# Performance work log

Measured on AMD Instinct MI355X. Metric: run time of the kernel, lower is better.

## Reference

```python
import jax, jax.numpy as jnp
import numpy as np

B, T, D, H = 4, 4096, 1024, 1024

def log_g(x):
    # log of g(x) = where(x>=0, x+0.5, sigmoid(x)), computed stably in log-space
    return jnp.where(x >= 0, jnp.log(jax.nn.relu(x) + 0.5), -jax.nn.softplus(-x))

def setup_inputs() -> dict:
    key = jax.random.key(0)
    ks = jax.random.split(key, 8)
    s = 1.0 / np.sqrt(D)
    return {
        "x":   jax.random.normal(ks[0], (B, T, D), dtype=jnp.float32),
        "h_0": jax.random.normal(ks[1], (B, H),    dtype=jnp.float32),
        "Wf":  jax.random.uniform(ks[2], (H, D), minval=-s, maxval=s, dtype=jnp.float32),
        "bf":  jax.random.uniform(ks[3], (H,),   minval=-s, maxval=s, dtype=jnp.float32),
        "Wi":  jax.random.uniform(ks[4], (H, D), minval=-s, maxval=s, dtype=jnp.float32),
        "bi":  jax.random.uniform(ks[5], (H,),   minval=-s, maxval=s, dtype=jnp.float32),
        "Wh":  jax.random.uniform(ks[6], (H, D), minval=-s, maxval=s, dtype=jnp.float32),
        "bh":  jax.random.uniform(ks[7], (H,),   minval=-s, maxval=s, dtype=jnp.float32),
    }

def reference(x, h_0, Wf, bf, Wi, bi, Wh, bh):
    # Gate pre-activations: (B, T, H)
    zf = jnp.einsum('btd,hd->bth', x, Wf) + bf
    zi = jnp.einsum('btd,hd->bth', x, Wi) + bi
    zh = jnp.einsum('btd,hd->bth', x, Wh) + bh

    # Normalized gates in log space: log f' = -softplus(diff), log i' = -softplus(-diff)
    diff = jax.nn.softplus(-zf) - jax.nn.softplus(-zi)
    log_f = -jax.nn.softplus(diff)
    log_i = -jax.nn.softplus(-diff)
    log_tilde_h = log_g(zh)

    log_h0 = log_g(h_0)[:, None, :]                               # (B, 1, H)
    log_values = jnp.concatenate([log_h0, log_i + log_tilde_h], axis=1)  # (B, T+1, H)

    # Log-space parallel scan: h_t = f_t h_{t-1} + v_t
    a_star = jnp.cumsum(log_f, axis=1)                            # (B, T, H)
    a_star_pad = jnp.pad(a_star, ((0, 0), (1, 0), (0, 0)))        # (B, T+1, H)
    log_h = a_star_pad + jax.lax.cumlogsumexp(log_values - a_star_pad, axis=1)
    return jnp.exp(log_h[:, 1:, :])                               # (B, T, H)
```

## Files before the change

### kernel.cpp

```cpp
#include <hip/hip_runtime.h>
#include <stdint.h>

#define BB 4
#define TT 4096
#define DD 1024
#define HH 1024
#define MM (BB * TT)
#define NC 128
#define CL (TT / NC)

typedef __bf16 bf16x8 __attribute__((ext_vector_type(8)));
typedef short  s16x8  __attribute__((ext_vector_type(8)));
typedef float  f32x4  __attribute__((ext_vector_type(4)));
typedef float  f32x16 __attribute__((ext_vector_type(16)));


__device__ __forceinline__ unsigned short f2bf(float f) {
    unsigned u = __float_as_uint(f);
    u += 0x7fffu + ((u >> 16) & 1u);
    return (unsigned short)(u >> 16);
}

__device__ __forceinline__ float bf2f(unsigned short u) {
    return __uint_as_float(((unsigned)u) << 16);
}

__device__ __forceinline__ float g_fn(float x) {
    return (x >= 0.f) ? (x + 0.5f) : 1.0f / (1.0f + __expf(-x));
}

__device__ __forceinline__ f32x16 mfma32(s16x8 a, s16x8 b, f32x16 c) {
    return __builtin_amdgcn_mfma_f32_32x32x16_bf16(
        __builtin_bit_cast(bf16x8, a), __builtin_bit_cast(bf16x8, b), c, 0, 0, 0);
}

__device__ __forceinline__ void async_copy16(const void* gsrc, void* ldst) {
    __builtin_amdgcn_global_load_lds(
        reinterpret_cast<__attribute__((address_space(1))) unsigned int*>(
            reinterpret_cast<uintptr_t>(gsrc)),
        reinterpret_cast<__attribute__((address_space(3))) unsigned int*>(
            reinterpret_cast<uintptr_t>(ldst)),
        16, 0, 0);
}


__global__ void cast_all(const float* __restrict__ x,
                         const float* __restrict__ Wf,
                         const float* __restrict__ Wi,
                         const float* __restrict__ Wh,
                         unsigned short* __restrict__ xb,
                         unsigned short* __restrict__ Wb) {
    const int NX = MM * DD / 4;
    int i = blockIdx.x * 256 + threadIdx.x;
    if (i < NX) {
        float4 v = reinterpret_cast<const float4*>(x)[i];
        ushort4 o;
        o.x = f2bf(v.x); o.y = f2bf(v.y); o.z = f2bf(v.z); o.w = f2bf(v.w);
        reinterpret_cast<ushort4*>(xb)[i] = o;
    } else {
        int j = i - NX;
        if (j < 3 * 262144) {
            int which = j >> 18, k = j & 262143;
            const float* s = (which == 0) ? Wf : ((which == 1) ? Wi : Wh);
            float4 v = reinterpret_cast<const float4*>(s)[k];
            ushort4 o;
            o.x = f2bf(v.x); o.y = f2bf(v.y); o.z = f2bf(v.z); o.w = f2bf(v.w);
            reinterpret_cast<ushort4*>(Wb)[(which << 18) + k] = o;
        }
    }
}


#define ISSUE(NB) do {                                                        \
    _Pragma("unroll")                                                         \
    for (int j = 0; j < 4; ++j)                                               \
        async_copy16(gptrA[j], smem + (NB) * 16384 + loffA[j]);               \
    _Pragma("unroll")                                                         \
    for (int j = 0; j < 3; ++j)                                               \
        async_copy16(gptrB[j], smem + 32768 + (NB) * 12288 + loffB[j]);       \
    _Pragma("unroll")                                                         \
    for (int j = 0; j < 4; ++j) gptrA[j] += 32;                               \
    _Pragma("unroll")                                                         \
    for (int j = 0; j < 3; ++j) gptrB[j] += 32;                               \
} while (0)

#define COMPUTE(CB) do {                                                      \
    const char* Ab = smem + (CB) * 16384;                                     \
    const char* Bb = smem + 32768 + (CB) * 12288;                             \
    _Pragma("unroll")                                                         \
    for (int ks = 0; ks < 2; ++ks) {                                          \
        const int col = c0 ^ (ks << 5);                                       \
        s16x8 a0 = *reinterpret_cast<const s16x8*>(Ab + arowb + col);         \
        s16x8 a1 = *reinterpret_cast<const s16x8*>(Ab + arowb + 2048 + col);  \
        s16x8 a2 = *reinterpret_cast<const s16x8*>(Ab + arowb + 4096 + col);  \
        s16x8 a3 = *reinterpret_cast<const s16x8*>(Ab + arowb + 6144 + col);  \
        s16x8 b0 = *reinterpret_cast<const s16x8*>(Bb + browb + col);         \
        s16x8 b1 = *reinterpret_cast<const s16x8*>(Bb + browb + 4096 + col);  \
        s16x8 b2 = *reinterpret_cast<const s16x8*>(Bb + browb + 8192 + col);  \
        acc[0][0] = mfma32(a0, b0, acc[0][0]);                                \
        acc[1][0] = mfma32(a0, b1, acc[1][0]);                                \
        acc[2][0] = mfma32(a0, b2, acc[2][0]);                                \
        acc[0][1] = mfma32(a1, b0, acc[0][1]);                                \
        acc[1][1] = mfma32(a1, b1, acc[1][1]);                                \
        acc[2][1] = mfma32(a1, b2, acc[2][1]);                                \
        acc[0][2] = mfma32(a2, b0, acc[0][2]);                                \
        acc[1][2] = mfma32(a2, b1, acc[1][2]);                                \
        acc[2][2] = mfma32(a2, b2, acc[2][2]);                                \
        acc[0][3] = mfma32(a3, b0, acc[0][3]);                                \
        acc[1][3] = mfma32(a3, b1, acc[1][3]);                                \
        acc[2][3] = mfma32(a3, b2, acc[2][3]);                                \
    }                                                                         \
} while (0)

#define STEP(CB, NB, LAST) do {                                               \
    if (!(LAST)) {                                                            \
        ISSUE(NB);                                                            \
        asm volatile("s_waitcnt vmcnt(7)" ::: "memory");                      \
    } else {                                                                  \
        asm volatile("s_waitcnt vmcnt(0)" ::: "memory");                      \
    }                                                                         \
    __builtin_amdgcn_s_barrier();                                             \
    COMPUTE(CB);                                                              \
    asm volatile("s_waitcnt lgkmcnt(0)" ::: "memory");                        \
    __builtin_amdgcn_s_barrier();                                             \
} while (0)

__global__ __launch_bounds__(256, 2) void gemm_gates(
    const unsigned short* __restrict__ xb,
    const unsigned short* __restrict__ Wb,
    const float* __restrict__ bf_p, const float* __restrict__ bi_p,
    const float* __restrict__ bh_p,
    unsigned short* __restrict__ F, unsigned short* __restrict__ V) {
    __shared__ char smem[57344];

    const int tid  = threadIdx.x;
    const int wave = tid >> 6;
    const int lane = tid & 63;

    const int bi  = blockIdx.x;
    const int xcd = bi & 7;
    const int jj  = bi >> 3;
    const int bm  = ((jj & 7) << 3) | xcd;
    const int bh  = jj >> 3;

    const int pm   = wave >> 1;
    const int ph   = wave & 1;

    const unsigned short* gptrA[4];
    const unsigned short* gptrB[3];
    int loffA[4], loffB[3];
#pragma unroll
    for (int j = 0; j < 4; ++j) {
        int s = wave + j * 4;
        int gch = (lane & 3) ^ ((lane >> 3) & 3) ^ ((s * 2 + (lane >> 5)) & 3);
        int row = bm * 256 + s * 16 + (lane >> 2);
        gptrA[j] = xb + (size_t)row * DD + gch * 8;
        loffA[j] = s * 1024;
    }
#pragma unroll
    for (int j = 0; j < 3; ++j) {
        int s = wave + j * 4;
        int gch = (lane & 3) ^ ((lane >> 3) & 3) ^ ((s * 2 + (lane >> 5)) & 3);
        int row = (s >> 2) * HH + bh * 64 + (s & 3) * 16 + (lane >> 2);
        gptrB[j] = Wb + (size_t)row * DD + gch * 8;
        loffB[j] = s * 1024;
    }

    const int c0 = (((lane >> 5) ^ ((lane >> 1) & 3) ^ ((lane >> 3) & 3)) << 4);
    const int arowb = (pm * 128 + (lane & 31)) * 64;
    const int browb = (ph * 32 + (lane & 31)) * 64;

    f32x16 acc[3][4];
#pragma unroll
    for (int g = 0; g < 3; ++g)
#pragma unroll
        for (int mt = 0; mt < 4; ++mt)
            acc[g][mt] = (f32x16)(0.f);

    ISSUE(0);
    for (int t = 0; t < 15; ++t) {
        STEP(0, 1, 0);
        STEP(1, 0, 0);
    }
    STEP(0, 1, 0);
    STEP(1, 0, 1);

    const int h   = bh * 64 + ph * 32 + (lane & 31);
    const float bfs = bf_p[h], bis = bi_p[h], bhs = bh_p[h];
    const int mb  = bm * 256 + pm * 128 + ((lane >> 5) << 2);
#pragma unroll
    for (int mt = 0; mt < 4; ++mt) {
#pragma unroll
        for (int r = 0; r < 16; ++r) {
            const int m = mb + mt * 32 + (r & 3) + ((r >> 2) << 3);
            float zf = acc[0][mt][r] + bfs;
            float zi = acc[1][mt][r] + bis;
            float zh = acc[2][mt][r] + bhs;
            float ea = __expf(fminf(-zf, 60.f));
            float eb = __expf(fminf(-zi, 60.f));
            float s  = __builtin_amdgcn_rcpf(2.f + ea + eb);
            float fv = (1.f + eb) * s;
            float iv = (1.f + ea) * s;
            float gg = (zh >= 0.f) ? (zh + 0.5f)
                                   : __builtin_amdgcn_rcpf(1.f + __expf(-zh));
            size_t o = (size_t)m * HH + h;
            F[o] = f2bf(fv);
            V[o] = f2bf(iv * gg);
        }
    }
}


__global__ void scan1_kernel(const unsigned short* __restrict__ F,
                             const unsigned short* __restrict__ V,
                             float* __restrict__ Fc, float* __restrict__ Vc) {
    const int bx = blockIdx.x, tid = threadIdx.x;
    const int c = bx & (NC - 1), b = bx >> 7;
    const ushort4* F4 = (const ushort4*)F;
    const ushort4* V4 = (const ushort4*)V;
    size_t base = ((size_t)(b * TT + c * CL) * HH) / 4 + tid;
    float4 Fp = {1.f, 1.f, 1.f, 1.f}, hv = {0.f, 0.f, 0.f, 0.f};
#pragma unroll 8
    for (int s = 0; s < CL; ++s) {
        ushort4 fu = F4[base + (size_t)s * (HH / 4)];
        ushort4 vu = V4[base + (size_t)s * (HH / 4)];
        hv.x = fmaf(bf2f(fu.x), hv.x, bf2f(vu.x)); Fp.x *= bf2f(fu.x);
        hv.y = fmaf(bf2f(fu.y), hv.y, bf2f(vu.y)); Fp.y *= bf2f(fu.y);
        hv.z = fmaf(bf2f(fu.z), hv.z, bf2f(vu.z)); Fp.z *= bf2f(fu.z);
        hv.w = fmaf(bf2f(fu.w), hv.w, bf2f(vu.w)); Fp.w *= bf2f(fu.w);
    }
    size_t ci = ((size_t)(b * NC + c) * HH) / 4 + tid;
    ((float4*)Fc)[ci] = Fp;
    ((float4*)Vc)[ci] = hv;
}

__global__ void scan2_kernel(const float* __restrict__ h0,
                             const float* __restrict__ Fc,
                             const float* __restrict__ Vc,
                             float* __restrict__ Hin) {
    const int gid = blockIdx.x * 256 + threadIdx.x;
    const int b = gid >> 10, h = gid & (HH - 1);
    float carry = g_fn(h0[gid]);
#pragma unroll 8
    for (int c = 0; c < NC; ++c) {
        int ci = (b * NC + c) * HH + h;
        Hin[ci] = carry;
        carry = fmaf(Fc[ci], carry, Vc[ci]);
    }
}

__global__ void scan3_kernel(const unsigned short* __restrict__ F,
                             const unsigned short* __restrict__ V,
                             const float* __restrict__ Hin,
                             float* __restrict__ Out) {
    const int bx = blockIdx.x, tid = threadIdx.x;
    const int c = bx & (NC - 1), b = bx >> 7;
    const ushort4* F4 = (const ushort4*)F;
    const ushort4* V4 = (const ushort4*)V;
    float4* O4 = (float4*)Out;
    size_t base = ((size_t)(b * TT + c * CL) * HH) / 4 + tid;
    size_t ci = ((size_t)(b * NC + c) * HH) / 4 + tid;
    float4 carry = ((const float4*)Hin)[ci];
#pragma unroll 8
    for (int s = 0; s < CL; ++s) {
        size_t idx = base + (size_t)s * (HH / 4);
        ushort4 fu = F4[idx];
        ushort4 vu = V4[idx];
        carry.x = fmaf(bf2f(fu.x), carry.x, bf2f(vu.x));
        carry.y = fmaf(bf2f(fu.y), carry.y, bf2f(vu.y));
        carry.z = fmaf(bf2f(fu.z), carry.z, bf2f(vu.z));
        carry.w = fmaf(bf2f(fu.w), carry.w, bf2f(vu.w));
        O4[idx] = carry;
    }
}


extern "C" void kernel_launch(void* const* d_in, const int* in_sizes, int n_in,
                              void* d_out, int out_size, void* d_ws, size_t ws_size,
                              hipStream_t stream) {
    const float* x   = (const float*)d_in[0];
    const float* h0  = (const float*)d_in[1];
    const float* Wf  = (const float*)d_in[2];
    const float* bfp = (const float*)d_in[3];
    const float* Wi  = (const float*)d_in[4];
    const float* bip = (const float*)d_in[5];
    const float* Wh  = (const float*)d_in[6];
    const float* bhp = (const float*)d_in[7];
    float* out = (float*)d_out;

    char* ws = (char*)d_ws;
    unsigned short* xb = (unsigned short*)ws;
    unsigned short* Wb = (unsigned short*)(ws + 33554432);
    unsigned short* Fb = (unsigned short*)(ws + 39845888);
    unsigned short* Vb = (unsigned short*)(ws + 73400320);
    float* Fc  = (float*)(ws);
    float* Vc  = (float*)(ws + 2097152);
    float* Hin = (float*)(ws + 4194304);

    cast_all<<<19456, 256, 0, stream>>>(x, Wf, Wi, Wh, xb, Wb);
    gemm_gates<<<1024, 256, 0, stream>>>(xb, Wb, bfp, bip, bhp, Fb, Vb);
    scan1_kernel<<<BB * NC, 256, 0, stream>>>(Fb, Vb, Fc, Vc);
    scan2_kernel<<<16, 256, 0, stream>>>(h0, Fc, Vc, Hin);
    scan3_kernel<<<BB * NC, 256, 0, stream>>>(Fb, Vb, Hin, out);
}
```

Before: 288.6 us.

## Restructure GEMM main loop to one barrier per stage with prefetch after sync

The double-buffered GEMM loop now waits for all outstanding loads, takes a single barrier, and only then issues the next stage's async copies into the other buffer, dropping the second barrier and the lgkmcnt wait per step. The compute body is manually unrolled so the second k-slice's A fragments are loaded ahead and its B fragments are loaded between the MFMA groups. s_setprio raises wave priority around the MFMA bursts. This cuts synchronisation overhead, at the cost of less load/compute overlap within a step because vmcnt(0) now waits for the just-issued prefetch before the next stage.

```diff
diff --git a/kernel.cpp b/kernel.cpp
--- a/kernel.cpp
+++ b/kernel.cpp
@@ -87,42 +87,57 @@
 #define COMPUTE(CB) do {                                                      \
     const char* Ab = smem + (CB) * 16384;                                     \
     const char* Bb = smem + 32768 + (CB) * 12288;                             \
-    _Pragma("unroll")                                                         \
-    for (int ks = 0; ks < 2; ++ks) {                                          \
-        const int col = c0 ^ (ks << 5);                                       \
-        s16x8 a0 = *reinterpret_cast<const s16x8*>(Ab + arowb + col);         \
-        s16x8 a1 = *reinterpret_cast<const s16x8*>(Ab + arowb + 2048 + col);  \
-        s16x8 a2 = *reinterpret_cast<const s16x8*>(Ab + arowb + 4096 + col);  \
-        s16x8 a3 = *reinterpret_cast<const s16x8*>(Ab + arowb + 6144 + col);  \
-        s16x8 b0 = *reinterpret_cast<const s16x8*>(Bb + browb + col);         \
-        s16x8 b1 = *reinterpret_cast<const s16x8*>(Bb + browb + 4096 + col);  \
-        s16x8 b2 = *reinterpret_cast<const s16x8*>(Bb + browb + 8192 + col);  \
-        acc[0][0] = mfma32(a0, b0, acc[0][0]);                                \
-        acc[1][0] = mfma32(a0, b1, acc[1][0]);                                \
-        acc[2][0] = mfma32(a0, b2, acc[2][0]);                                \
-        acc[0][1] = mfma32(a1, b0, acc[0][1]);                                \
-        acc[1][1] = mfma32(a1, b1, acc[1][1]);                                \
-        acc[2][1] = mfma32(a1, b2, acc[2][1]);                                \
-        acc[0][2] = mfma32(a2, b0, acc[0][2]);                                \
-        acc[1][2] = mfma32(a2, b1, acc[1][2]);                                \
-        acc[2][2] = mfma32(a2, b2, acc[2][2]);                                \
-        acc[0][3] = mfma32(a3, b0, acc[0][3]);                                \
-        acc[1][3] = mfma32(a3, b1, acc[1][3]);                                \
-        acc[2][3] = mfma32(a3, b2, acc[2][3]);                                \
-    }                                                                         \
+    const int c1 = c0 ^ 32;                                                   \
+    s16x8 a0 = *reinterpret_cast<const s16x8*>(Ab + arowb + c0);              \
+    s16x8 a1 = *reinterpret_cast<const s16x8*>(Ab + arowb + 2048 + c0);       \
+    s16x8 a2 = *reinterpret_cast<const s16x8*>(Ab + arowb + 4096 + c0);       \
+    s16x8 a3 = *reinterpret_cast<const s16x8*>(Ab + arowb + 6144 + c0);       \
+    s16x8 b0 = *reinterpret_cast<const s16x8*>(Bb + browb + c0);              \
+    s16x8 b1 = *reinterpret_cast<const s16x8*>(Bb + browb + 4096 + c0);       \
+    s16x8 b2 = *reinterpret_cast<const s16x8*>(Bb + browb + 8192 + c0);       \
+    s16x8 A0 = *reinterpret_cast<const s16x8*>(Ab + arowb + c1);              \
+    s16x8 A1 = *reinterpret_cast<const s16x8*>(Ab + arowb + 2048 + c1);       \
+    s16x8 A2 = *reinterpret_cast<const s16x8*>(Ab + arowb + 4096 + c1);       \
+    s16x8 A3 = *reinterpret_cast<const s16x8*>(Ab + arowb + 6144 + c1);       \
+    __builtin_amdgcn_s_setprio(1);                                            \
+    acc[0][0] = mfma32(a0, b0, acc[0][0]);                                    \
+    acc[1][0] = mfma32(a0, b1, acc[1][0]);                                    \
+    acc[2][0] = mfma32(a0, b2, acc[2][0]);                                    \
+    acc[0][1] = mfma32(a1, b0, acc[0][1]);                                    \
+    acc[1][1] = mfma32(a1, b1, acc[1][1]);                                    \
+    acc[2][1] = mfma32(a1, b2, acc[2][1]);                                    \
+    acc[0][2] = mfma32(a2, b0, acc[0][2]);                                    \
+    acc[1][2] = mfma32(a2, b1, acc[1][2]);                                    \
+    acc[2][2] = mfma32(a2, b2, acc[2][2]);                                    \
+    acc[0][3] = mfma32(a3, b0, acc[0][3]);                                    \
+    acc[1][3] = mfma32(a3, b1, acc[1][3]);                                    \
+    acc[2][3] = mfma32(a3, b2, acc[2][3]);                                    \
+    __builtin_amdgcn_s_setprio(0);                                            \
+    s16x8 B0 = *reinterpret_cast<const s16x8*>(Bb + browb + c1);              \
+    s16x8 B1 = *reinterpret_cast<const s16x8*>(Bb + browb + 4096 + c1);       \
+    s16x8 B2 = *reinterpret_cast<const s16x8*>(Bb + browb + 8192 + c1);       \
+    __builtin_amdgcn_s_setprio(1);                                            \
+    acc[0][0] = mfma32(A0, B0, acc[0][0]);                                    \
+    acc[1][0] = mfma32(A0, B1, acc[1][0]);                                    \
+    acc[2][0] = mfma32(A0, B2, acc[2][0]);                                    \
+    acc[0][1] = mfma32(A1, B0, acc[0][1]);                                    \
+    acc[1][1] = mfma32(A1, B1, acc[1][1]);                                    \
+    acc[2][1] = mfma32(A1, B2, acc[2][1]);                                    \
+    acc[0][2] = mfma32(A2, B0, acc[0][2]);                                    \
+    acc[1][2] = mfma32(A2, B1, acc[1][2]);                                    \
+    acc[2][2] = mfma32(A2, B2, acc[2][2]);                                    \
+    acc[0][3] = mfma32(A3, B0, acc[0][3]);                                    \
+    acc[1][3] = mfma32(A3, B1, acc[1][3]);                                    \
+    acc[2][3] = mfma32(A3, B2, acc[2][3]);                                    \
+    __builtin_amdgcn_s_setprio(0);                                            \
 } while (0)
 
-#define STEP(CB, NB, LAST) do {                                               \
-    if (!(LAST)) {                                                            \
-        ISSUE(NB);                                                            \
-        asm volatile("s_waitcnt vmcnt(7)" ::: "memory");                      \
-    } else {                                                                  \
-        asm volatile("s_waitcnt vmcnt(0)" ::: "memory");                      \
-    }                                                                         \
+#define STEP(CB, NB, DO_ISSUE) do {                                           \
+    asm volatile("s_waitcnt vmcnt(0)" ::: "memory");                          \
     __builtin_amdgcn_s_barrier();                                             \
+    asm volatile("" ::: "memory");                                            \
+    if (DO_ISSUE) ISSUE(NB);                                                  \
     COMPUTE(CB);                                                              \
-    asm volatile("s_waitcnt lgkmcnt(0)" ::: "memory");                        \
-    __builtin_amdgcn_s_barrier();                                             \
 } while (0)
 
 __global__ __launch_bounds__(256, 2) void gemm_gates(
@@ -179,11 +194,11 @@
 
     ISSUE(0);
     for (int t = 0; t < 15; ++t) {
-        STEP(0, 1, 0);
-        STEP(1, 0, 0);
-    }
-    STEP(0, 1, 0);
-    STEP(1, 0, 1);
+        STEP(0, 1, 1);
+        STEP(1, 0, 1);
+    }
+    STEP(0, 1, 1);
+    STEP(1, 0, 0);
 
     const int h   = bh * 64 + ph * 32 + (lane & 31);
     const float bfs = bf_p[h], bis = bi_p[h], bhs = bh_p[h];
```

Result: slower. 616.4 us (+113.6%).
